# Kernel tuning notes

Hardware: AMD Instinct MI355X
Metric: run time of the kernel (lower is better)

## Reference

```python
import jax, jax.numpy as jnp
import numpy as np

NIBBLES_PER_I32 = 8


def unpack_int4(q):
    """Unpack int32 [..., n] -> uint4 values in int32 [..., n*8], LSB-first."""
    shifts = (jnp.arange(NIBBLES_PER_I32, dtype=jnp.int32) * 4)
    nib = (q[..., None] >> shifts) & 0xF  # [..., n, 8]
    return nib.reshape(q.shape[:-1] + (q.shape[-1] * NIBBLES_PER_I32,))


def setup_inputs() -> dict:
    key = jax.random.key(0)
    k_x, k_w, k_z, k_s, k_b = jax.random.split(key, 5)
    B, S, IN, OUT, G = 2, 4096, 4096, 4096, 32
    x = jax.random.normal(k_x, (B, S, IN), dtype=jnp.float16)
    qweight = jax.random.randint(k_w, (OUT, IN // 8), 0, 2147483647, dtype=jnp.int32)
    qzeros = jax.random.randint(k_z, (G, OUT // 8), 0, 2147483647, dtype=jnp.int32)
    scales = (jax.random.uniform(k_s, (G, OUT), dtype=jnp.float32) * 0.01 + 0.001).astype(jnp.float16)
    bias = (jax.random.normal(k_b, (OUT,), dtype=jnp.float32) * 0.01).astype(jnp.float16)
    return {"x": x, "qweight": qweight, "qzeros": qzeros, "scales": scales, "bias": bias}


def reference(x, qweight, qzeros, scales, bias):
    # GPTQ W4A16: dequantize int4 weight with per-group scales/zero-points, then GEMM + bias.
    x = x.astype(jnp.float16)
    wq = unpack_int4(qweight)            # [out, in] int4 values
    zq = unpack_int4(qzeros)             # [groups, out]
    out_f, in_f = wq.shape
    G = scales.shape[0]
    gsize = in_f // G
    wq_g = wq.reshape(out_f, G, gsize)                       # [out, G, gsize]
    zero = zq.T.astype(jnp.float16)[:, :, None]              # [out, G, 1]
    scale = scales.T.astype(jnp.float16)[:, :, None]         # [out, G, 1]
    w = ((wq_g.astype(jnp.float16) - zero) * scale).reshape(out_f, in_f)  # [out, in] fp16
    y = jnp.einsum("bsi,oi->bso", x, w)                     # [B, S, out]
    return y + bias
```

## Files before the change

kernel.cpp:

```cpp
#include <hip/hip_runtime.h>
#include <cstdint>

typedef unsigned short u16;
typedef unsigned int   u32;
typedef unsigned long long u64;

typedef _Float16 f16x2 __attribute__((ext_vector_type(2)));
typedef _Float16 f16x8 __attribute__((ext_vector_type(8)));
typedef float    f32x4 __attribute__((ext_vector_type(4)));

__device__ __forceinline__ u32 cvt_pk(float a, float b) {
    return __builtin_bit_cast(u32, __builtin_amdgcn_cvt_pkrtz(a, b));
}

__device__ __forceinline__ f16x8 unpack_dq(u32 q, f16x2 cz, f16x2 cs) {
    const u32 b0 = (q & 0x000F000Fu) | 0x64006400u;
    const u32 b1 = ((q >> 4) & 0x000F000Fu) | 0x64006400u;
    const u32 b2 = ((q >> 8) & 0x000F000Fu) | 0x64006400u;
    const u32 b3 = ((q >> 12) & 0x000F000Fu) | 0x64006400u;
    const f16x2 w0 = (__builtin_bit_cast(f16x2, b0) - cz) * cs;
    const f16x2 w1 = (__builtin_bit_cast(f16x2, b1) - cz) * cs;
    const f16x2 w2 = (__builtin_bit_cast(f16x2, b2) - cz) * cs;
    const f16x2 w3 = (__builtin_bit_cast(f16x2, b3) - cz) * cs;
    uint4 w;
    w.x = __builtin_bit_cast(u32, w0);
    w.y = __builtin_bit_cast(u32, w1);
    w.z = __builtin_bit_cast(u32, w2);
    w.w = __builtin_bit_cast(u32, w3);
    return __builtin_bit_cast(f16x8, w);
}

__device__ __forceinline__ void load_lds16(const void* g, void* l) {
    __builtin_amdgcn_global_load_lds(
        (const __attribute__((address_space(1))) void*)g,
        (__attribute__((address_space(3))) void*)l,
        16, 0, 0);
}

__global__ __launch_bounds__(256) void gptq_prepass(
    const float* __restrict__ X, u16* __restrict__ Xh)
{
    const u32 gid = blockIdx.x * 256 + threadIdx.x;
    const u32 m  = gid >> 9;
    const u32 kg = gid & 511;
    const float* src = X + ((u64)m << 12) + kg * 8;
    const float4 f0 = *(const float4*)src;
    const float4 f1 = *(const float4*)(src + 4);
    uint4 w;
    w.x = cvt_pk(f0.x, f1.x);
    w.y = cvt_pk(f0.y, f1.y);
    w.z = cvt_pk(f0.z, f1.z);
    w.w = cvt_pk(f0.w, f1.w);
    const u32 mt = m >> 7, r = m & 127, t = kg >> 3, g = kg & 7;
    *(uint4*)(Xh + (((u64)mt * 64 + t) << 13) + r * 64 + ((g ^ (r & 7)) * 8)) = w;
}

__global__ __launch_bounds__(256, 2) void gptq_gemm_dma(
    const u16* __restrict__ Xh,
    const int* __restrict__ QW,
    const int* __restrict__ QZ,
    const float* __restrict__ SC,
    const float* __restrict__ BIAS,
    float* __restrict__ Y)
{
    constexpr int N = 4096, KB = 512, NT = 64;

    __shared__ __align__(16) u16 Alds[2][128 * 64];

    const int tid  = threadIdx.x;
    const int lane = tid & 63;
    const int wid  = tid >> 6;

    const int mt = blockIdx.x;
    const int m0 = mt * 128;
    const int n0 = blockIdx.y * 256;

    f32x4 acc[8][4];
#pragma unroll
    for (int i = 0; i < 8; i++)
#pragma unroll
        for (int j = 0; j < 4; j++)
            acc[i][j] = (f32x4){0.f, 0.f, 0.f, 0.f};

    const int fr   = lane & 15;
    const int quad = lane >> 4;
    const int fr7  = fr & 7;

    const char* xsrc = (const char*)Xh + (((u64)mt * NT) << 14)
                     + wid * 4096 + lane * 16;

    const int nbase = n0 + wid * 64 + fr;
    const char* QWb = (const char*)QW;
    u32 qoff[4];
#pragma unroll
    for (int ni = 0; ni < 4; ni++)
        qoff[ni] = (u32)(((nbase + ni * 16) * KB + quad * 2) * 4);
    const int zsh = fr7 * 4;

    int2  bq[2][4];
    float sf_st[4];
    int   zw_st[4];
    f16x2 cs[4], cz[4];

    auto STAGE = [&](int buf, int t) {
        const char* s = xsrc + ((u64)t << 14);
        char* d = (char*)&Alds[buf][0] + wid * 4096;
#pragma unroll
        for (int i = 0; i < 4; i++)
            load_lds16(s + i * 1024, d + i * 1024);
    };

    auto FETCH_B = [&](int t, int nb) {
        const u32 tb = (u32)t * 32;
#pragma unroll
        for (int ni = 0; ni < 4; ni++)
            bq[nb][ni] = *(const int2*)(QWb + qoff[ni] + tb);
    };

    auto FETCH_SZ = [&](int g) {
#pragma unroll
        for (int ni = 0; ni < 4; ni++) {
            sf_st[ni] = SC[g * N + nbase + ni * 16];
            zw_st[ni] = QZ[g * (N / 8) + ((nbase + ni * 16) >> 3)];
        }
    };

    auto CONV_SZ = [&]() {
#pragma unroll
        for (int ni = 0; ni < 4; ni++) {
            const int z = (zw_st[ni] >> zsh) & 0xF;
            const _Float16 hs = (_Float16)sf_st[ni];
            const _Float16 hz = (_Float16)(float)(1024 + z);
            cs[ni] = (f16x2){hs, hs};
            cz[ni] = (f16x2){hz, hz};
        }
    };

    auto COMPUTE = [&](int buf, int nb) {
#pragma unroll
        for (int ks = 0; ks < 2; ks++) {
            f16x8 bfr[4];
#pragma unroll
            for (int ni = 0; ni < 4; ni++) {
                const u32 q = (u32)(ks == 0 ? bq[nb][ni].x : bq[nb][ni].y);
                bfr[ni] = unpack_dq(q, cz[ni], cs[ni]);
            }
            const int gsw = ((quad * 2 + ks) ^ fr7) * 8;
#pragma unroll
            for (int mi = 0; mi < 8; mi++) {
                const f16x8 af =
                    *(const f16x8*)(&Alds[buf][(mi * 16 + fr) * 64 + gsw]);
#pragma unroll
                for (int ni = 0; ni < 4; ni++)
                    acc[mi][ni] = __builtin_amdgcn_mfma_f32_16x16x32_f16(
                        af, bfr[ni], acc[mi][ni], 0, 0, 0);
            }
        }
    };

    STAGE(0, 0);
    FETCH_B(0, 0);
    FETCH_SZ(0);
    CONV_SZ();
    asm volatile("s_waitcnt vmcnt(0)" ::: "memory");
    __syncthreads();

    for (int t = 0; t < NT; t += 2) {
        STAGE(1, t + 1);
        FETCH_B(t + 1, 1);
        COMPUTE(0, 0);
        asm volatile("s_waitcnt vmcnt(0)" ::: "memory");
        __syncthreads();

        const bool last = (t + 2 >= NT);
        if (!last) {
            STAGE(0, t + 2);
            FETCH_B(t + 2, 0);
            FETCH_SZ((t + 2) >> 1);
        }
        COMPUTE(1, 1);
        if (!last) CONV_SZ();
        asm volatile("s_waitcnt vmcnt(0)" ::: "memory");
        __syncthreads();
    }

    const int cn  = lane & 15;
    const int q4r = quad * 4;
#pragma unroll
    for (int ni = 0; ni < 4; ni++) {
        const int col = n0 + wid * 64 + ni * 16 + cn;
        const float bz = BIAS[col];
#pragma unroll
        for (int mi = 0; mi < 8; mi++) {
            const int rbase = m0 + mi * 16 + q4r;
#pragma unroll
            for (int r = 0; r < 4; r++) {
                Y[(u64)(rbase + r) * N + col] = acc[mi][ni][r] + bz;
            }
        }
    }
}

__global__ __launch_bounds__(256, 2) void gptq_gemm_fb(
    const float* __restrict__ X, const int* __restrict__ QW,
    const int* __restrict__ QZ, const float* __restrict__ SC,
    const float* __restrict__ BIAS, float* __restrict__ Y)
{
    constexpr int N = 4096, K = 4096, KB = 512, NT = 64;
    __shared__ __align__(16) u16 Alds[2][128 * 64];
    __shared__ __align__(16) u16 Blds[2][128 * 64];

    const int tid = threadIdx.x, lane = tid & 63, wid = tid >> 6;
    const int m0 = blockIdx.x * 128, n0 = blockIdx.y * 128;

    f32x4 acc[4][4];
#pragma unroll
    for (int i = 0; i < 4; i++)
#pragma unroll
        for (int j = 0; j < 4; j++) acc[i][j] = (f32x4){0.f, 0.f, 0.f, 0.f};

    const int wm = (wid >> 1) * 64, wn = (wid & 1) * 64;
    const int lrowA = tid >> 3, lcolA = (tid & 7) * 8;
    const float* gA = X + (u64)(m0 + lrowA) * K + lcolA;
    const int sA = ((tid & 7) ^ (lrowA & 7)) * 8;
    const int nl = tid >> 1, kq0 = (tid & 1) * 4;
    const int nglob = n0 + nl;
    const int* qrow = QW + (u64)nglob * KB;
    const int nl7 = nl & 7, zsh = (nglob & 7) * 4;
    const float* scp = SC + nglob;
    const int* qzp = QZ + (nglob >> 3);
    const int fr = lane & 15, quad = lane >> 4, fr7 = fr & 7;

    float4 af32[8];
    int4 q4;
    float sf;
    int zw;

    auto FETCH = [&](int t) {
        const int kt = t * 64;
#pragma unroll
        for (int i = 0; i < 4; i++) {
            const float* pa = gA + (u64)i * 32 * K + kt;
            af32[2 * i] = *(const float4*)pa;
            af32[2 * i + 1] = *(const float4*)(pa + 4);
        }
        q4 = *(const int4*)(qrow + (kt >> 3) + kq0);
        const int g = t >> 1;
        sf = scp[g * N];
        zw = qzp[g * (N / 8)];
    };
    auto STORE = [&](int buf) {
#pragma unroll
        for (int i = 0; i < 4; i++) {
            const float4 f0 = af32[2 * i], f1 = af32[2 * i + 1];
            uint4 w;
            w.x = cvt_pk(f0.x, f1.x); w.y = cvt_pk(f0.y, f1.y);
            w.z = cvt_pk(f0.z, f1.z); w.w = cvt_pk(f0.w, f1.w);
            *(uint4*)(&Alds[buf][(i * 32 + lrowA) * 64 + sA]) = w;
        }
        const int z = (zw >> zsh) & 0xF;
        const _Float16 hs = (_Float16)sf;
        const _Float16 hz = (_Float16)(float)(1024 + z);
        const f16x2 cs2 = {hs, hs}, cz2 = {hz, hz};
        const int qv[4] = {q4.x, q4.y, q4.z, q4.w};
#pragma unroll
        for (int c = 0; c < 4; c++) {
            const f16x8 wv = unpack_dq((u32)qv[c], cz2, cs2);
            const int gran = ((kq0 + c) ^ nl7) * 8;
            *(f16x8*)(&Blds[buf][nl * 64 + gran]) = wv;
        }
    };
    auto COMPUTE = [&](int buf) {
#pragma unroll
        for (int ks = 0; ks < 2; ks++) {
            const int gsw = ((ks * 4 + quad) ^ fr7) * 8;
            f16x8 af[4], bfr[4];
#pragma unroll
            for (int i = 0; i < 4; i++)
                af[i] = *(const f16x8*)(&Alds[buf][(wm + i * 16 + fr) * 64 + gsw]);
#pragma unroll
            for (int i = 0; i < 4; i++)
                bfr[i] = *(const f16x8*)(&Blds[buf][(wn + i * 16 + fr) * 64 + gsw]);
#pragma unroll
            for (int mi = 0; mi < 4; mi++)
#pragma unroll
                for (int ni = 0; ni < 4; ni++)
                    acc[mi][ni] = __builtin_amdgcn_mfma_f32_16x16x32_f16(
                        af[mi], bfr[ni], acc[mi][ni], 0, 0, 0);
        }
    };

    FETCH(0); STORE(0); __syncthreads();
#pragma unroll 2
    for (int t = 0; t < NT; ++t) {
        const int cur = t & 1;
        if (t + 1 < NT) FETCH(t + 1);
        COMPUTE(cur);
        if (t + 1 < NT) STORE(cur ^ 1);
        __syncthreads();
    }
    const int cn = lane & 15, q4r = quad * 4;
#pragma unroll
    for (int ni = 0; ni < 4; ni++) {
        const int col = n0 + wn + ni * 16 + cn;
        const float bz = BIAS[col];
#pragma unroll
        for (int mi = 0; mi < 4; mi++) {
            const int rbase = m0 + wm + mi * 16 + q4r;
#pragma unroll
            for (int r = 0; r < 4; r++)
                Y[(u64)(rbase + r) * N + col] = acc[mi][ni][r] + bz;
        }
    }
}

extern "C" void kernel_launch(void* const* d_in, const int* in_sizes, int n_in,
                              void* d_out, int out_size, void* d_ws, size_t ws_size,
                              hipStream_t stream) {
    const float* X    = (const float*)d_in[0];
    const int*   QW   = (const int*)d_in[1];
    const int*   QZ   = (const int*)d_in[2];
    const float* SC   = (const float*)d_in[3];
    const float* BIAS = (const float*)d_in[4];
    float* Y = (float*)d_out;

    const size_t need = (size_t)8192 * 4096 * sizeof(u16);
    if (ws_size >= need) {
        u16* Xh = (u16*)d_ws;
        gptq_prepass<<<16384, 256, 0, stream>>>(X, Xh);
        dim3 grid(64, 16, 1);
        gptq_gemm_dma<<<grid, 256, 0, stream>>>(Xh, QW, QZ, SC, BIAS, Y);
    } else {
        dim3 grid(64, 32, 1);
        gptq_gemm_fb<<<grid, 256, 0, stream>>>(X, QW, QZ, SC, BIAS, Y);
    }
}
```

Measured before the change: 525.2 us.

## Deepen GEMM pipeline with split barriers, tile-ordered prepass, and MFMA priority

The main GEMM loop now keeps two A tiles in flight. It replaces the full vmcnt(0) waits plus __syncthreads with partial s_waitcnt counts and raw s_barrier, so global-to-LDS DMA and weight fetches can overlap with compute. The weight fetch switches from one int2 per row to two strided int32 loads, which changes the k-interleave so each lane reads contiguous nibble words in a different order. MFMA sections are wrapped in s_setprio. The prepass is restructured so each block writes one contiguous swizzled tile, with 4096 blocks of 4 passes. The hand-counted vmcnt values are fragile and could race if the compiler reorders loads.

```diff
diff --git a/kernel.cpp b/kernel.cpp
--- a/kernel.cpp
+++ b/kernel.cpp
@@ -40,19 +40,24 @@
 __global__ __launch_bounds__(256) void gptq_prepass(
     const float* __restrict__ X, u16* __restrict__ Xh)
 {
-    const u32 gid = blockIdx.x * 256 + threadIdx.x;
-    const u32 m  = gid >> 9;
-    const u32 kg = gid & 511;
-    const float* src = X + ((u64)m << 12) + kg * 8;
-    const float4 f0 = *(const float4*)src;
-    const float4 f1 = *(const float4*)(src + 4);
-    uint4 w;
-    w.x = cvt_pk(f0.x, f1.x);
-    w.y = cvt_pk(f0.y, f1.y);
-    w.z = cvt_pk(f0.z, f1.z);
-    w.w = cvt_pk(f0.w, f1.w);
-    const u32 mt = m >> 7, r = m & 127, t = kg >> 3, g = kg & 7;
-    *(uint4*)(Xh + (((u64)mt * 64 + t) << 13) + r * 64 + ((g ^ (r & 7)) * 8)) = w;
+    const u32 tile = blockIdx.x;
+    const u32 mt = tile >> 6, t = tile & 63;
+    const float* bsrc = X + ((u64)mt << 19) + t * 64;
+    u16* bdst = Xh + ((u64)tile << 13);
+#pragma unroll
+    for (int pass = 0; pass < 4; ++pass) {
+        const u32 idx = pass * 256 + threadIdx.x;
+        const u32 r = idx >> 3, sg = idx & 7, g = sg ^ (r & 7);
+        const float* s = bsrc + ((u64)r << 12) + g * 8;
+        const float4 f0 = *(const float4*)s;
+        const float4 f1 = *(const float4*)(s + 4);
+        uint4 w;
+        w.x = cvt_pk(f0.x, f1.x);
+        w.y = cvt_pk(f0.y, f1.y);
+        w.z = cvt_pk(f0.z, f1.z);
+        w.w = cvt_pk(f0.w, f1.w);
+        *(uint4*)(bdst + idx * 8) = w;
+    }
 }
 
 __global__ __launch_bounds__(256, 2) void gptq_gemm_dma(
@@ -94,10 +99,10 @@
     u32 qoff[4];
 #pragma unroll
     for (int ni = 0; ni < 4; ni++)
-        qoff[ni] = (u32)(((nbase + ni * 16) * KB + quad * 2) * 4);
+        qoff[ni] = (u32)(((nbase + ni * 16) * KB + quad) * 4);
     const int zsh = fr7 * 4;
 
-    int2  bq[2][4];
+    int   bq[2][8];
     float sf_st[4];
     int   zw_st[4];
     f16x2 cs[4], cz[4];
@@ -113,8 +118,10 @@
     auto FETCH_B = [&](int t, int nb) {
         const u32 tb = (u32)t * 32;
 #pragma unroll
-        for (int ni = 0; ni < 4; ni++)
-            bq[nb][ni] = *(const int2*)(QWb + qoff[ni] + tb);
+        for (int ni = 0; ni < 4; ni++) {
+            bq[nb][ni * 2 + 0] = *(const int*)(QWb + qoff[ni] + tb);
+            bq[nb][ni * 2 + 1] = *(const int*)(QWb + qoff[ni] + tb + 16);
+        }
     };
 
     auto FETCH_SZ = [&](int g) {
@@ -141,11 +148,10 @@
         for (int ks = 0; ks < 2; ks++) {
             f16x8 bfr[4];
 #pragma unroll
-            for (int ni = 0; ni < 4; ni++) {
-                const u32 q = (u32)(ks == 0 ? bq[nb][ni].x : bq[nb][ni].y);
-                bfr[ni] = unpack_dq(q, cz[ni], cs[ni]);
-            }
-            const int gsw = ((quad * 2 + ks) ^ fr7) * 8;
+            for (int ni = 0; ni < 4; ni++)
+                bfr[ni] = unpack_dq((u32)bq[nb][ni * 2 + ks], cz[ni], cs[ni]);
+            const int gsw = ((ks * 4 + quad) ^ fr7) * 8;
+            __builtin_amdgcn_s_setprio(1);
 #pragma unroll
             for (int mi = 0; mi < 8; mi++) {
                 const f16x8 af =
@@ -155,34 +161,37 @@
                     acc[mi][ni] = __builtin_amdgcn_mfma_f32_16x16x32_f16(
                         af, bfr[ni], acc[mi][ni], 0, 0, 0);
             }
-        }
-    };
-
-    STAGE(0, 0);
+            __builtin_amdgcn_s_setprio(0);
+        }
+    };
+
     FETCH_B(0, 0);
     FETCH_SZ(0);
+    STAGE(0, 0);
+    STAGE(1, 1);
     CONV_SZ();
-    asm volatile("s_waitcnt vmcnt(0)" ::: "memory");
-    __syncthreads();
-
-    for (int t = 0; t < NT; t += 2) {
-        STAGE(1, t + 1);
+    asm volatile("s_waitcnt vmcnt(4)\n\ts_barrier" ::: "memory");
+
+    for (int t = 0; t <= 60; t += 2) {
         FETCH_B(t + 1, 1);
+        FETCH_SZ((t >> 1) + 1);
         COMPUTE(0, 0);
-        asm volatile("s_waitcnt vmcnt(0)" ::: "memory");
-        __syncthreads();
-
-        const bool last = (t + 2 >= NT);
-        if (!last) {
-            STAGE(0, t + 2);
-            FETCH_B(t + 2, 0);
-            FETCH_SZ((t + 2) >> 1);
-        }
+        asm volatile("s_barrier" ::: "memory");
+        STAGE(0, t + 2);
+        asm volatile("s_waitcnt vmcnt(20)\n\ts_barrier" ::: "memory");
+
+        FETCH_B(t + 2, 0);
         COMPUTE(1, 1);
-        if (!last) CONV_SZ();
-        asm volatile("s_waitcnt vmcnt(0)" ::: "memory");
-        __syncthreads();
-    }
+        CONV_SZ();
+        asm volatile("s_barrier" ::: "memory");
+        STAGE(1, t + 3);
+        asm volatile("s_waitcnt vmcnt(12)\n\ts_barrier" ::: "memory");
+    }
+
+    FETCH_B(63, 1);
+    COMPUTE(0, 0);
+    asm volatile("s_waitcnt vmcnt(8)\n\ts_barrier" ::: "memory");
+    COMPUTE(1, 1);
 
     const int cn  = lane & 15;
     const int q4r = quad * 4;
@@ -220,8 +229,8 @@
         for (int j = 0; j < 4; j++) acc[i][j] = (f32x4){0.f, 0.f, 0.f, 0.f};
 
     const int wm = (wid >> 1) * 64, wn = (wid & 1) * 64;
-    const int lrowA = tid >> 3, lcolA = (tid & 7) * 8;
-    const float* gA = X + (u64)(m0 + lrowA) * K + lcolA;
+    const int lrowA = tid >> 3;
+    const float* gA = X + (u64)(m0 + lrowA) * K + (tid & 7) * 8;
     const int sA = ((tid & 7) ^ (lrowA & 7)) * 8;
     const int nl = tid >> 1, kq0 = (tid & 1) * 4;
     const int nglob = n0 + nl;
@@ -327,7 +336,7 @@
     const size_t need = (size_t)8192 * 4096 * sizeof(u16);
     if (ws_size >= need) {
         u16* Xh = (u16*)d_ws;
-        gptq_prepass<<<16384, 256, 0, stream>>>(X, Xh);
+        gptq_prepass<<<4096, 256, 0, stream>>>(X, Xh);
         dim3 grid(64, 16, 1);
         gptq_gemm_dma<<<grid, 256, 0, stream>>>(Xh, QW, QZ, SC, BIAS, Y);
     } else {
```

New measurement: 581.1 us. +10.6%, slower.
